# Kernel optimization log

Measured on AMD Instinct MI355X. Metric: run time of the kernel, lower is better.

## Reference

```python
import jax, jax.numpy as jnp
import numpy as np

EPS = 1e-5

def _fftfreq(n, d):
    k = jnp.concatenate([jnp.arange(0, (n + 1) // 2), jnp.arange(-(n // 2), 0)]).astype(jnp.float32)
    return k / (n * d)

def _inorm(x):
    # InstanceNorm2d, no affine, biased variance, eps=1e-5; x: (B,C,H,W)
    m = jnp.mean(x, axis=(-2, -1), keepdims=True)
    v = jnp.var(x, axis=(-2, -1), keepdims=True)
    return (x - m) / jnp.sqrt(v + EPS)

def _spectral_conv(x, t_grid, x_grid, p1, p2, res):
    # x: (B, C, Sx, Sy) real; p1:(in,out,m1) p2:(in,out,m2) res:(in,out,m1,m2) complex64
    B, C, Sx, Sy = x.shape
    dty = x_grid[0, 1] - x_grid[0, 0]
    dtx = t_grid[0, 1] - t_grid[0, 0]
    alpha = jnp.fft.fft2(x, axes=(-2, -1))  # (B,in,Sx,Sy) complex
    om1 = (_fftfreq(Sx, dty) * (2 * jnp.pi) * 1j).astype(jnp.complex64)  # (Sx,)
    om2 = (_fftfreq(Sy, dtx) * (2 * jnp.pi) * 1j).astype(jnp.complex64)  # (Sy,)
    d1 = om1[:, None, None, None] - p1  # (Sx,in,out,m1)
    d2 = om2[:, None, None, None] - p2  # (Sy,in,out,m2)
    denom = jnp.einsum('pbix,qbik->pqbixk', d1, d2)  # (Sx,Sy,in,out,m1,m2)
    Hw = res[None, None] / denom  # pole-residue rational kernel
    r1 = jnp.einsum('biox,oxikpq->bkox', alpha, Hw)  # (B,out,Sx,Sy)
    r2 = jnp.einsum('biox,oxikpq->bkpq', alpha, Hw)  # (B,out,m1,m2)
    x1 = jnp.real(jnp.fft.ifft2(r1, s=(Sx, Sy), axes=(-2, -1)))
    ty_c = x_grid.reshape(1, -1).astype(jnp.complex64)  # (1,Sx)
    tx_c = t_grid.reshape(1, -1).astype(jnp.complex64)  # (1,Sy)
    e1 = jnp.exp(jnp.einsum('bip,kz->bipz', p1, ty_c))  # (in,out,m1,Sx)
    e2 = jnp.exp(jnp.einsum('biq,kx->biqx', p2, tx_c))  # (in,out,m2,Sy)
    term3 = jnp.einsum('bipz,biqx->bipqzx', e1, e2)     # (in,out,m1,m2,Sx,Sy)
    x2 = jnp.real(jnp.einsum('kbpq,bipqzx->kizx', r2, term3)) / (Sx * Sy)
    return x1 + x2

def reference(x, fc0_w, fc0_b, p1r, p1i, p2r, p2i, resr, resi,
              w0_w, w0_b, fc1_w, fc1_b, fc2_w, fc2_b, t_grid, x_grid):
    B, Sx, Sy, _ = x.shape
    gx = jnp.broadcast_to(jnp.linspace(0.0, 1.0, Sx, dtype=jnp.float32)[None, :, None, None], (B, Sx, Sy, 1))
    gy = jnp.broadcast_to(jnp.linspace(0.0, 1.0, Sy, dtype=jnp.float32)[None, None, :, None], (B, Sx, Sy, 1))
    h = jnp.concatenate([x, gx, gy], axis=-1)           # (B,Sx,Sy,3)
    h = h @ fc0_w.T + fc0_b                              # (B,Sx,Sy,16)
    h = h.transpose(0, 3, 1, 2)                          # (B,16,Sx,Sy)
    p1 = (p1r + 1j * p1i).astype(jnp.complex64)
    p2 = (p2r + 1j * p2i).astype(jnp.complex64)
    res = (resr + 1j * resi).astype(jnp.complex64)
    x1 = _inorm(_spectral_conv(_inorm(h), t_grid, x_grid, p1, p2, res))
    x2 = jnp.einsum('bihw,oi->bohw', h, w0_w) + w0_b[None, :, None, None]  # 1x1 conv
    h = x1 + x2
    h = h.transpose(0, 2, 3, 1)                          # (B,Sx,Sy,16)
    h = jnp.sin(h @ fc1_w.T + fc1_b)                     # (B,Sx,Sy,128)
    h = h @ fc2_w.T + fc2_b                              # (B,Sx,Sy,1)
    return h

def setup_inputs() -> dict:
    key = jax.random.key(0)
    ks = jax.random.split(key, 16)
    W, M1, M2, B, S = 16, 4, 5, 4, 64
    scale = 1.0 / (W * W)
    inp = {
        'x': jax.random.normal(ks[0], (B, S, S, 1), jnp.float32),
        'fc0_w': jax.random.normal(ks[1], (W, 3), jnp.float32) * 0.3,
        'fc0_b': jax.random.normal(ks[2], (W,), jnp.float32) * 0.1,
        'p1r': jax.random.uniform(ks[3], (W, W, M1), jnp.float32) * scale,
        'p1i': jax.random.uniform(ks[4], (W, W, M1), jnp.float32) * scale,
        'p2r': jax.random.uniform(ks[5], (W, W, M2), jnp.float32) * scale,
        'p2i': jax.random.uniform(ks[6], (W, W, M2), jnp.float32) * scale,
        'resr': jax.random.uniform(ks[7], (W, W, M1, M2), jnp.float32) * scale,
        'resi': jax.random.uniform(ks[8], (W, W, M1, M2), jnp.float32) * scale,
        'w0_w': jax.random.normal(ks[9], (W, W), jnp.float32) * 0.25,
        'w0_b': jax.random.normal(ks[10], (W,), jnp.float32) * 0.1,
        'fc1_w': jax.random.normal(ks[11], (128, W), jnp.float32) * 0.25,
        'fc1_b': jax.random.normal(ks[12], (128,), jnp.float32) * 0.1,
        'fc2_w': jax.random.normal(ks[13], (1, 128), jnp.float32) * 0.1,
        'fc2_b': jax.random.normal(ks[14], (1,), jnp.float32) * 0.1,
        't_grid': jnp.linspace(0.0, 1.0, S, dtype=jnp.float32).reshape(1, S),
        'x_grid': jnp.linspace(0.0, 1.0, S, dtype=jnp.float32).reshape(1, S),
    }
    return inp
```

## Files before the change

kernel.cpp:

```cpp
#include <hip/hip_runtime.h>

typedef float2 cplx;

constexpr float TWO_PI = 6.28318530717958647692f;

__device__ inline void cmac(float& ax, float& ay, cplx a, cplx b) {
    ax += a.x * b.x - a.y * b.y;
    ay += a.x * b.y + a.y * b.x;
}

__global__ __launch_bounds__(256) void k_pre(
    const float* __restrict__ x, const float* __restrict__ fc0_w,
    const float* __restrict__ fc0_b,
    const float* __restrict__ p1r, const float* __restrict__ p1i,
    const float* __restrict__ p2r, const float* __restrict__ p2i,
    const float* __restrict__ resr, const float* __restrict__ resi,
    const float* __restrict__ t_grid, const float* __restrict__ x_grid,
    cplx* __restrict__ A, cplx* __restrict__ Bq, cplx* __restrict__ Cq,
    cplx* __restrict__ e1, cplx* __restrict__ e2,
    float* __restrict__ h, float* __restrict__ accH)
{
    int idx = blockIdx.x * 256 + threadIdx.x;
    float dty = x_grid[1] - x_grid[0];
    float dtx = t_grid[1] - t_grid[0];
    const int NA = 65536, NBQ = 81920, NCQ = 81920, NE1 = 65536, NE2 = 81920;
    if (idx < NA) {
        int p = idx & 3, k = (idx >> 2) & 15, i = (idx >> 6) & 15, o = idx >> 10;
        int kf = (o < 32) ? o : o - 64;
        float om = TWO_PI * (float)kf / (64.f * dty);
        float dr = -p1r[(i * 16 + k) * 4 + p], di = om - p1i[(i * 16 + k) * 4 + p];
        float inv = 1.f / (dr * dr + di * di);
        A[idx] = make_float2(dr * inv, -di * inv);
        return;
    }
    idx -= NA;
    if (idx < NBQ) {
        int q = idx % 5, k = (idx / 5) & 15, i = (idx / 80) & 15, xx = idx / 1280;
        int kf = (xx < 32) ? xx : xx - 64;
        float om = TWO_PI * (float)kf / (64.f * dtx);
        float dr = -p2r[(i * 16 + k) * 5 + q], di = om - p2i[(i * 16 + k) * 5 + q];
        float inv = 1.f / (dr * dr + di * di);
        Bq[idx] = make_float2(dr * inv, -di * inv);
        return;
    }
    idx -= NBQ;
    if (idx < NCQ) {
        int q = idx % 5, k = (idx / 5) & 15, i = (idx / 80) & 15, o = idx / 1280;
        int kf = (o < 32) ? o : o - 64;
        float om = TWO_PI * (float)kf / (64.f * dty);
        float cx = 0.f, cy = 0.f;
        for (int p = 0; p < 4; ++p) {
            float dr = -p1r[(i * 16 + k) * 4 + p], di = om - p1i[(i * 16 + k) * 4 + p];
            float inv = 1.f / (dr * dr + di * di);
            float axr = dr * inv, axi = -di * inv;
            float rr = resr[((i * 16 + k) * 4 + p) * 5 + q];
            float ri = resi[((i * 16 + k) * 4 + p) * 5 + q];
            cx += rr * axr - ri * axi;
            cy += rr * axi + ri * axr;
        }
        Cq[idx] = make_float2(cx, cy);
        return;
    }
    idx -= NCQ;
    if (idx < NE1) {
        int z = idx & 63, w = idx >> 6;
        float t = x_grid[z];
        float m = expf(p1r[w] * t);
        float sn, cs; sincosf(p1i[w] * t, &sn, &cs);
        e1[idx] = make_float2(m * cs, m * sn);
        return;
    }
    idx -= NE1;
    if (idx < NE2) {
        int xx = idx & 63, w = idx >> 6;
        float t = t_grid[xx];
        float m = expf(p2r[w] * t);
        float sn, cs; sincosf(p2i[w] * t, &sn, &cs);
        e2[idx] = make_float2(m * cs, m * sn);
        return;
    }
    idx -= NE2;
    {
        int bc = idx >> 12, pix = idx & 4095;
        int b = bc >> 4, c = bc & 15;
        int z = pix >> 6, xx = pix & 63;
        const float inv63 = 1.f / 63.f;
        float v = fc0_w[c * 3] * x[b * 4096 + pix]
                + fc0_w[c * 3 + 1] * (z * inv63)
                + fc0_w[c * 3 + 2] * (xx * inv63) + fc0_b[c];
        h[idx] = v;
        float s = v, s2 = v * v;
        for (int m = 32; m; m >>= 1) {
            s  += __shfl_xor(s,  m, 64);
            s2 += __shfl_xor(s2, m, 64);
        }
        if ((threadIdx.x & 63) == 0) {
            atomicAdd(&accH[bc * 2],     s);
            atomicAdd(&accH[bc * 2 + 1], s2);
        }
    }
}

__global__ __launch_bounds__(256) void k_fftA(
    const float* __restrict__ h, const float* __restrict__ accH,
    cplx* __restrict__ T1)
{
    __shared__ cplx Ws[64];
    int bc = blockIdx.x >> 4, pc = blockIdx.x & 15;
    int tid = threadIdx.x;
    if (tid < 64) { float sn, cs; sincosf(-TWO_PI * tid / 64.f, &sn, &cs); Ws[tid] = make_float2(cs, sn); }
    __syncthreads();
    float mean = accH[bc * 2] * (1.f / 4096.f);
    float var  = accH[bc * 2 + 1] * (1.f / 4096.f) - mean * mean;
    float rstd = rsqrtf(var + 1e-5f);
    int j = tid & 63, pl = tid >> 6, p = pc * 4 + pl;
    const float* hb = h + bc * 4096 + j;
    float ax = 0.f, ay = 0.f;
    #pragma unroll 8
    for (int i = 0; i < 64; ++i) {
        float v = hb[i * 64];
        cplx w = Ws[(p * i) & 63];
        ax += v * w.x; ay += v * w.y;
    }
    if (p == 0) ax -= 64.f * mean;
    T1[bc * 4096 + p * 64 + j] = make_float2(ax * rstd, ay * rstd);
}

__global__ __launch_bounds__(256) void k2_fftB(
    const cplx* __restrict__ T1, cplx* __restrict__ alpha, cplx* __restrict__ alphaT)
{
    __shared__ cplx T1s[256];
    int bc = blockIdx.x >> 4, pc = blockIdx.x & 15;
    int tid = threadIdx.x;
    T1s[tid] = T1[bc * 4096 + pc * 256 + tid];
    __syncthreads();
    int q = tid & 63, pl = tid >> 6, p = pc * 4 + pl;
    float c1, s1; sincosf(-TWO_PI * (float)q * (1.f / 64.f), &s1, &c1);
    float wx = 1.f, wy = 0.f;
    float ax = 0.f, ay = 0.f;
    #pragma unroll 8
    for (int j = 0; j < 64; ++j) {
        cplx t = T1s[pl * 64 + j];
        ax += t.x * wx - t.y * wy;
        ay += t.x * wy + t.y * wx;
        float nwx = wx * c1 - wy * s1;
        wy = wx * s1 + wy * c1; wx = nwx;
    }
    cplx v = make_float2(ax, ay);
    alpha [bc * 4096 + p * 64 + q] = v;
    alphaT[(p * 64 + q) * 64 + bc] = v;
}

__global__ __launch_bounds__(64) void k3_r1(
    const cplx* __restrict__ alphaT, const cplx* __restrict__ Cq,
    const cplx* __restrict__ Bq, cplx* __restrict__ r1)
{
    __shared__ cplx Cqs[1280], Bqs[1280], Gs[256], as[64];
    int ox = blockIdx.x; int o = ox >> 6, xx = ox & 63;
    int t = threadIdx.x;
    for (int m = 0; m < 20; ++m) {
        Cqs[m * 64 + t] = Cq[o * 1280 + m * 64 + t];
        Bqs[m * 64 + t] = Bq[xx * 1280 + m * 64 + t];
    }
    as[t] = alphaT[ox * 64 + t];
    __syncthreads();
    for (int m = 0; m < 4; ++m) {
        int e = m * 64 + t; int i = e >> 4, k = e & 15;
        float gx = 0.f, gy = 0.f;
        for (int q = 0; q < 5; ++q) cmac(gx, gy, Cqs[i * 80 + k * 5 + q], Bqs[i * 80 + k * 5 + q]);
        Gs[e] = make_float2(gx, gy);
    }
    __syncthreads();
    int b = t >> 4, k = t & 15;
    float ax = 0.f, ay = 0.f;
    for (int i = 0; i < 16; ++i) cmac(ax, ay, as[b * 16 + i], Gs[i * 16 + k]);
    r1[t * 4096 + ox] = make_float2(ax, ay);
}

__global__ __launch_bounds__(256) void k4_inner1(
    const cplx* __restrict__ alpha, const cplx* __restrict__ Bq,
    cplx* __restrict__ inner1)
{
    int idx = blockIdx.x * 256 + threadIdx.x;
    int kq = idx % 80; int r = idx / 80; int o = r & 63; int bi = r >> 6; int i = bi & 15;
    const cplx* arow = alpha + bi * 4096 + o * 64;
    const cplx* bcol = Bq + i * 80 + kq;
    float ax = 0.f, ay = 0.f;
    #pragma unroll 4
    for (int x = 0; x < 64; ++x) cmac(ax, ay, arow[x], bcol[x * 1280]);
    inner1[idx] = make_float2(ax, ay);
}

__global__ __launch_bounds__(256) void k5_r2(
    const cplx* __restrict__ A, const cplx* __restrict__ inner1,
    const float* __restrict__ resr, const float* __restrict__ resi,
    cplx* __restrict__ r2)
{
    __shared__ cplx red[4][20];
    int bk = blockIdx.x; int b = bk >> 4, k = bk & 15;
    int o = threadIdx.x & 63, ig = threadIdx.x >> 6;
    float accx[4][5] = {}, accy[4][5] = {};
    for (int ii = 0; ii < 4; ++ii) {
        int i = ig * 4 + ii;
        cplx a[4];
        for (int p = 0; p < 4; ++p) a[p] = A[((o * 16 + i) * 16 + k) * 4 + p];
        cplx in[5];
        for (int q = 0; q < 5; ++q) in[q] = inner1[(b * 16 + i) * 5120 + o * 80 + k * 5 + q];
        int rb = (i * 16 + k) * 20;
        for (int p = 0; p < 4; ++p)
            for (int q = 0; q < 5; ++q) {
                float tx = a[p].x * in[q].x - a[p].y * in[q].y;
                float ty = a[p].x * in[q].y + a[p].y * in[q].x;
                float rr = resr[rb + p * 5 + q], ri = resi[rb + p * 5 + q];
                accx[p][q] += rr * tx - ri * ty;
                accy[p][q] += rr * ty + ri * tx;
            }
    }
    for (int m = 32; m; m >>= 1)
        for (int p = 0; p < 4; ++p)
            for (int q = 0; q < 5; ++q) {
                accx[p][q] += __shfl_xor(accx[p][q], m, 64);
                accy[p][q] += __shfl_xor(accy[p][q], m, 64);
            }
    if (o == 0)
        for (int p = 0; p < 4; ++p)
            for (int q = 0; q < 5; ++q)
                red[ig][p * 5 + q] = make_float2(accx[p][q], accy[p][q]);
    __syncthreads();
    if (threadIdx.x < 20) {
        float sx = 0.f, sy = 0.f;
        for (int g = 0; g < 4; ++g) { sx += red[g][threadIdx.x].x; sy += red[g][threadIdx.x].y; }
        r2[bk * 20 + threadIdx.x] = make_float2(sx, sy);
    }
}

__global__ __launch_bounds__(256) void k7_ifftA(
    const cplx* __restrict__ r1, cplx* __restrict__ T2)
{
    __shared__ cplx Ws[64];
    int bk = blockIdx.x >> 4, zc = blockIdx.x & 15;
    int tid = threadIdx.x;
    if (tid < 64) { float sn, cs; sincosf(TWO_PI * tid / 64.f, &sn, &cs); Ws[tid] = make_float2(cs, sn); }
    __syncthreads();
    int j = tid & 63, z = zc * 4 + (tid >> 6);
    const cplx* rr = r1 + bk * 4096 + j;
    float ax = 0.f, ay = 0.f;
    #pragma unroll 4
    for (int o = 0; o < 64; ++o) cmac(ax, ay, rr[o * 64], Ws[(z * o) & 63]);
    T2[bk * 4096 + z * 64 + j] = make_float2(ax, ay);
}

__global__ __launch_bounds__(256) void k8b_sp(
    const cplx* __restrict__ T2, const cplx* __restrict__ r2,
    const cplx* __restrict__ e1, const cplx* __restrict__ e2,
    float* __restrict__ sp, float* __restrict__ accS)
{
    __shared__ cplx Es[5120];
    __shared__ cplx Vs[320];
    __shared__ cplx T2s[256];
    int bc = blockIdx.x >> 4, zc = blockIdx.x & 15;
    int b = bc >> 4, ch = bc & 15;
    int tid = threadIdx.x;
    for (int t = 0; t < 20; ++t) {
        int f = t * 256 + tid;
        int bb = f / 320, r = f - bb * 320;
        Es[f] = e2[(bb * 16 + ch) * 320 + r];
    }
    T2s[tid] = T2[bc * 4096 + zc * 256 + tid];
    for (int e = tid; e < 320; e += 256) {
        int bq = e >> 2, zl = e & 3;
        int bb = bq / 5, q = bq - bb * 5;
        int z = zc * 4 + zl;
        float vx = 0.f, vy = 0.f;
        for (int p = 0; p < 4; ++p)
            cmac(vx, vy, r2[(b * 16 + bb) * 20 + p * 5 + q],
                         e1[((bb * 16 + ch) * 4 + p) * 64 + z]);
        Vs[e] = make_float2(vx, vy);
    }
    __syncthreads();
    int zl = tid >> 6, xx = tid & 63;
    float c1, s1; sincosf(TWO_PI * (float)xx * (1.f / 64.f), &s1, &c1);
    float wx = 1.f, wy = 0.f;
    float acc = 0.f;
    const cplx* trow = &T2s[zl * 64];
    #pragma unroll 8
    for (int j = 0; j < 64; ++j) {
        cplx t = trow[j];
        acc += t.x * wx - t.y * wy;
        float nwx = wx * c1 - wy * s1;
        wy = wx * s1 + wy * c1; wx = nwx;
    }
    #pragma unroll 5
    for (int bq = 0; bq < 80; ++bq) {
        cplx vv = Vs[bq * 4 + zl];
        cplx ee = Es[bq * 64 + xx];
        acc += vv.x * ee.x - vv.y * ee.y;
    }
    float val = acc * (1.f / 4096.f);
    sp[bc * 4096 + zc * 256 + tid] = val;
    float s = val, s2 = val * val;
    for (int m = 32; m; m >>= 1) {
        s  += __shfl_xor(s,  m, 64);
        s2 += __shfl_xor(s2, m, 64);
    }
    if ((tid & 63) == 0) {
        atomicAdd(&accS[bc * 2],     s);
        atomicAdd(&accS[bc * 2 + 1], s2);
    }
}

__global__ __launch_bounds__(256) void k9_final(
    const float* __restrict__ sp, const float* __restrict__ accS,
    const float* __restrict__ h,
    const float* __restrict__ w0_w, const float* __restrict__ w0_b,
    const float* __restrict__ fc1_w, const float* __restrict__ fc1_b,
    const float* __restrict__ fc2_w, const float* __restrict__ fc2_b,
    float* __restrict__ out)
{
    __shared__ float w1s[128 * 16], b1s[128], w2s[128], w0s[256], w0bs[16];
    __shared__ float mvm[16], mvr[16];
    int tid = threadIdx.x;
    int b = blockIdx.x >> 4;
    for (int t = 0; t < 8; ++t) w1s[t * 256 + tid] = fc1_w[t * 256 + tid];
    if (tid < 128) { b1s[tid] = fc1_b[tid]; w2s[tid] = fc2_w[tid]; }
    w0s[tid] = w0_w[tid & 255];
    if (tid < 16) {
        w0bs[tid] = w0_b[tid];
        float mean = accS[(b * 16 + tid) * 2] * (1.f / 4096.f);
        float var  = accS[(b * 16 + tid) * 2 + 1] * (1.f / 4096.f) - mean * mean;
        mvm[tid] = mean;
        mvr[tid] = rsqrtf(var + 1e-5f);
    }
    float b2 = fc2_b[0];
    __syncthreads();
    int pix = blockIdx.x * 256 + tid;
    int rem = pix & 4095;
    float hv[16], tv[16];
    for (int c = 0; c < 16; ++c) {
        hv[c] = h[(b * 16 + c) * 4096 + rem];
        tv[c] = (sp[(b * 16 + c) * 4096 + rem] - mvm[c]) * mvr[c];
    }
    for (int k = 0; k < 16; ++k) {
        float a = w0bs[k];
        for (int c = 0; c < 16; ++c) a += w0s[k * 16 + c] * hv[c];
        tv[k] += a;
    }
    float acc = b2;
    for (int n = 0; n < 128; ++n) {
        float s1 = b1s[n];
        for (int k2 = 0; k2 < 16; ++k2) s1 += w1s[n * 16 + k2] * tv[k2];
        acc += w2s[n] * sinf(s1);
    }
    out[pix] = acc;
}

extern "C" void kernel_launch(void* const* d_in, const int* in_sizes, int n_in,
                              void* d_out, int out_size, void* d_ws, size_t ws_size,
                              hipStream_t stream)
{
    const float* x     = (const float*)d_in[0];
    const float* fc0_w = (const float*)d_in[1];
    const float* fc0_b = (const float*)d_in[2];
    const float* p1r   = (const float*)d_in[3];
    const float* p1i   = (const float*)d_in[4];
    const float* p2r   = (const float*)d_in[5];
    const float* p2i   = (const float*)d_in[6];
    const float* resr  = (const float*)d_in[7];
    const float* resi  = (const float*)d_in[8];
    const float* w0_w  = (const float*)d_in[9];
    const float* w0_b  = (const float*)d_in[10];
    const float* fc1_w = (const float*)d_in[11];
    const float* fc1_b = (const float*)d_in[12];
    const float* fc2_w = (const float*)d_in[13];
    const float* fc2_b = (const float*)d_in[14];
    const float* t_grid= (const float*)d_in[15];
    const float* x_grid= (const float*)d_in[16];
    float* out = (float*)d_out;

    float* ws = (float*)d_ws;
    size_t off = 0;
    float* h      = ws + off; off += 262144;
    cplx*  T1     = (cplx*)(ws + off); off += 524288;
    cplx*  alpha  = (cplx*)(ws + off); off += 524288;
    cplx*  alphaT = (cplx*)(ws + off); off += 524288;
    cplx*  A      = (cplx*)(ws + off); off += 131072;
    cplx*  Bq     = (cplx*)(ws + off); off += 163840;
    cplx*  Cq     = (cplx*)(ws + off); off += 163840;
    cplx*  e1     = (cplx*)(ws + off); off += 131072;
    cplx*  e2     = (cplx*)(ws + off); off += 163840;
    cplx*  r1     = (cplx*)(ws + off); off += 524288;
    cplx*  inner1 = (cplx*)(ws + off); off += 655360;
    cplx*  r2     = (cplx*)(ws + off); off += 2560;
    cplx*  T2     = (cplx*)(ws + off); off += 524288;
    float* sp     = ws + off; off += 262144;
    float* accum  = ws + off; off += 256;
    float* accH = accum, *accS = accum + 128;
    (void)ws_size; (void)n_in; (void)in_sizes; (void)out_size;

    hipMemsetAsync(accum, 0, 256 * sizeof(float), stream);

    k_pre<<<2496, 256, 0, stream>>>(x, fc0_w, fc0_b, p1r, p1i, p2r, p2i, resr, resi,
                                    t_grid, x_grid, A, Bq, Cq, e1, e2, h, accH);
    k_fftA<<<1024, 256, 0, stream>>>(h, accH, T1);
    k2_fftB<<<1024, 256, 0, stream>>>(T1, alpha, alphaT);
    k3_r1<<<4096, 64, 0, stream>>>(alphaT, Cq, Bq, r1);
    k4_inner1<<<1280, 256, 0, stream>>>(alpha, Bq, inner1);
    k5_r2<<<64, 256, 0, stream>>>(A, inner1, resr, resi, r2);
    k7_ifftA<<<1024, 256, 0, stream>>>(r1, T2);
    k8b_sp<<<1024, 256, 0, stream>>>(T2, r2, e1, e2, sp, accS);
    k9_final<<<64, 256, 0, stream>>>(sp, accS, h, w0_w, w0_b, fc1_w, fc1_b, fc2_w, fc2_b, out);
}
```

Measured before the change: 251.6 us.

## Replace stat atomics with per-wave partials and read e2 directly from global

Instance-norm sum/sum-of-squares accumulation now writes per-wave partials to distinct slots instead of atomicAdd, and the consumer kernels reduce them with wave shuffles. This removes the memset launch and atomic contention. The spectral reconstruction kernel also stops staging the e2 table in 40KB of shared memory and reads it from global memory/cache instead. This frees LDS for occupancy at the cost of more global loads.

```diff
diff --git a/kernel.cpp b/kernel.cpp
--- a/kernel.cpp
+++ b/kernel.cpp
@@ -18,7 +18,7 @@
     const float* __restrict__ t_grid, const float* __restrict__ x_grid,
     cplx* __restrict__ A, cplx* __restrict__ Bq, cplx* __restrict__ Cq,
     cplx* __restrict__ e1, cplx* __restrict__ e2,
-    float* __restrict__ h, float* __restrict__ accH)
+    float* __restrict__ h, float* __restrict__ accH2)
 {
     int idx = blockIdx.x * 256 + threadIdx.x;
     float dty = x_grid[1] - x_grid[0];
@@ -95,24 +95,35 @@
             s2 += __shfl_xor(s2, m, 64);
         }
         if ((threadIdx.x & 63) == 0) {
-            atomicAdd(&accH[bc * 2],     s);
-            atomicAdd(&accH[bc * 2 + 1], s2);
+            int widx = pix >> 6;
+            accH2[bc * 128 + widx * 2]     = s;
+            accH2[bc * 128 + widx * 2 + 1] = s2;
         }
     }
 }
 
 __global__ __launch_bounds__(256) void k_fftA(
-    const float* __restrict__ h, const float* __restrict__ accH,
+    const float* __restrict__ h, const float* __restrict__ accH2,
     cplx* __restrict__ T1)
 {
     __shared__ cplx Ws[64];
+    __shared__ float mv[2];
     int bc = blockIdx.x >> 4, pc = blockIdx.x & 15;
     int tid = threadIdx.x;
     if (tid < 64) { float sn, cs; sincosf(-TWO_PI * tid / 64.f, &sn, &cs); Ws[tid] = make_float2(cs, sn); }
-    __syncthreads();
-    float mean = accH[bc * 2] * (1.f / 4096.f);
-    float var  = accH[bc * 2 + 1] * (1.f / 4096.f) - mean * mean;
-    float rstd = rsqrtf(var + 1e-5f);
+    if (tid >= 64 && tid < 128) {
+        int l = tid - 64;
+        float s  = accH2[bc * 128 + l * 2];
+        float s2 = accH2[bc * 128 + l * 2 + 1];
+        for (int m = 32; m; m >>= 1) { s += __shfl_xor(s, m, 64); s2 += __shfl_xor(s2, m, 64); }
+        if (l == 0) {
+            float mean = s * (1.f / 4096.f);
+            float var  = s2 * (1.f / 4096.f) - mean * mean;
+            mv[0] = mean; mv[1] = rsqrtf(var + 1e-5f);
+        }
+    }
+    __syncthreads();
+    float mean = mv[0], rstd = mv[1];
     int j = tid & 63, pl = tid >> 6, p = pc * 4 + pl;
     const float* hb = h + bc * 4096 + j;
     float ax = 0.f, ay = 0.f;
@@ -250,22 +261,16 @@
     T2[bk * 4096 + z * 64 + j] = make_float2(ax, ay);
 }
 
-__global__ __launch_bounds__(256) void k8b_sp(
+__global__ __launch_bounds__(256) void k8c_sp(
     const cplx* __restrict__ T2, const cplx* __restrict__ r2,
     const cplx* __restrict__ e1, const cplx* __restrict__ e2,
-    float* __restrict__ sp, float* __restrict__ accS)
-{
-    __shared__ cplx Es[5120];
+    float* __restrict__ sp, float* __restrict__ accS2)
+{
     __shared__ cplx Vs[320];
     __shared__ cplx T2s[256];
     int bc = blockIdx.x >> 4, zc = blockIdx.x & 15;
     int b = bc >> 4, ch = bc & 15;
     int tid = threadIdx.x;
-    for (int t = 0; t < 20; ++t) {
-        int f = t * 256 + tid;
-        int bb = f / 320, r = f - bb * 320;
-        Es[f] = e2[(bb * 16 + ch) * 320 + r];
-    }
     T2s[tid] = T2[bc * 4096 + zc * 256 + tid];
     for (int e = tid; e < 320; e += 256) {
         int bq = e >> 2, zl = e & 3;
@@ -290,12 +295,14 @@
         float nwx = wx * c1 - wy * s1;
         wy = wx * s1 + wy * c1; wx = nwx;
     }
-    #pragma unroll 5
-    for (int bq = 0; bq < 80; ++bq) {
-        cplx vv = Vs[bq * 4 + zl];
-        cplx ee = Es[bq * 64 + xx];
-        acc += vv.x * ee.x - vv.y * ee.y;
-    }
+    const cplx* eb = e2 + ch * 320 + xx;
+    #pragma unroll 4
+    for (int bb = 0; bb < 16; ++bb)
+        for (int q = 0; q < 5; ++q) {
+            cplx vv = Vs[(bb * 5 + q) * 4 + zl];
+            cplx ee = eb[bb * 5120 + q * 64];
+            acc += vv.x * ee.x - vv.y * ee.y;
+        }
     float val = acc * (1.f / 4096.f);
     sp[bc * 4096 + zc * 256 + tid] = val;
     float s = val, s2 = val * val;
@@ -304,13 +311,14 @@
         s2 += __shfl_xor(s2, m, 64);
     }
     if ((tid & 63) == 0) {
-        atomicAdd(&accS[bc * 2],     s);
-        atomicAdd(&accS[bc * 2 + 1], s2);
+        int widx = zc * 4 + (tid >> 6);
+        accS2[bc * 128 + widx * 2]     = s;
+        accS2[bc * 128 + widx * 2 + 1] = s2;
     }
 }
 
 __global__ __launch_bounds__(256) void k9_final(
-    const float* __restrict__ sp, const float* __restrict__ accS,
+    const float* __restrict__ sp, const float* __restrict__ accS2,
     const float* __restrict__ h,
     const float* __restrict__ w0_w, const float* __restrict__ w0_b,
     const float* __restrict__ fc1_w, const float* __restrict__ fc1_b,
@@ -324,12 +332,20 @@
     for (int t = 0; t < 8; ++t) w1s[t * 256 + tid] = fc1_w[t * 256 + tid];
     if (tid < 128) { b1s[tid] = fc1_b[tid]; w2s[tid] = fc2_w[tid]; }
     w0s[tid] = w0_w[tid & 255];
-    if (tid < 16) {
-        w0bs[tid] = w0_b[tid];
-        float mean = accS[(b * 16 + tid) * 2] * (1.f / 4096.f);
-        float var  = accS[(b * 16 + tid) * 2 + 1] * (1.f / 4096.f) - mean * mean;
-        mvm[tid] = mean;
-        mvr[tid] = rsqrtf(var + 1e-5f);
+    if (tid < 16) w0bs[tid] = w0_b[tid];
+    {
+        int wv = tid >> 6, ln = tid & 63;
+        for (int cc = 0; cc < 4; ++cc) {
+            int c = wv * 4 + cc;
+            float s  = accS2[(b * 16 + c) * 128 + ln * 2];
+            float s2 = accS2[(b * 16 + c) * 128 + ln * 2 + 1];
+            for (int m = 32; m; m >>= 1) { s += __shfl_xor(s, m, 64); s2 += __shfl_xor(s2, m, 64); }
+            if (ln == 0) {
+                float mean = s * (1.f / 4096.f);
+                float var  = s2 * (1.f / 4096.f) - mean * mean;
+                mvm[c] = mean; mvr[c] = rsqrtf(var + 1e-5f);
+            }
+        }
     }
     float b2 = fc2_b[0];
     __syncthreads();
@@ -393,20 +409,18 @@
     cplx*  r2     = (cplx*)(ws + off); off += 2560;
     cplx*  T2     = (cplx*)(ws + off); off += 524288;
     float* sp     = ws + off; off += 262144;
-    float* accum  = ws + off; off += 256;
-    float* accH = accum, *accS = accum + 128;
+    float* accH2  = ws + off; off += 8192;
+    float* accS2  = ws + off; off += 8192;
     (void)ws_size; (void)n_in; (void)in_sizes; (void)out_size;
 
-    hipMemsetAsync(accum, 0, 256 * sizeof(float), stream);
-
     k_pre<<<2496, 256, 0, stream>>>(x, fc0_w, fc0_b, p1r, p1i, p2r, p2i, resr, resi,
-                                    t_grid, x_grid, A, Bq, Cq, e1, e2, h, accH);
-    k_fftA<<<1024, 256, 0, stream>>>(h, accH, T1);
+                                    t_grid, x_grid, A, Bq, Cq, e1, e2, h, accH2);
+    k_fftA<<<1024, 256, 0, stream>>>(h, accH2, T1);
     k2_fftB<<<1024, 256, 0, stream>>>(T1, alpha, alphaT);
     k3_r1<<<4096, 64, 0, stream>>>(alphaT, Cq, Bq, r1);
     k4_inner1<<<1280, 256, 0, stream>>>(alpha, Bq, inner1);
     k5_r2<<<64, 256, 0, stream>>>(A, inner1, resr, resi, r2);
     k7_ifftA<<<1024, 256, 0, stream>>>(r1, T2);
-    k8b_sp<<<1024, 256, 0, stream>>>(T2, r2, e1, e2, sp, accS);
-    k9_final<<<64, 256, 0, stream>>>(sp, accS, h, w0_w, w0_b, fc1_w, fc1_b, fc2_w, fc2_b, out);
-}
+    k8c_sp<<<1024, 256, 0, stream>>>(T2, r2, e1, e2, sp, accS2);
+    k9_final<<<64, 256, 0, stream>>>(sp, accS2, h, w0_w, w0_b, fc1_w, fc1_b, fc2_w, fc2_b, out);
+}
```

Result: faster. 202.5 us (-19.5%).
